# Performance work log

Hardware: AMD Instinct MI355X
Metric: run time of the kernel (lower is better)

## Reference

```python
import jax, jax.numpy as jnp
import numpy as np

B, N, C, R, E = 8, 4096, 128, 16, 65536


def setup_inputs() -> dict:
    key = jax.random.key(0)
    ks = jax.random.split(key, 8)
    node_features = jax.random.normal(ks[0], (B, N, C), dtype=jnp.float32)
    edge_index = jax.random.randint(ks[1], (B, 2, E), 0, N, dtype=jnp.int64)
    edge_type = jax.random.randint(ks[2], (B, E), 0, R, dtype=jnp.int64)
    s = 1.0 / np.sqrt(C)
    rel_weight = jax.random.uniform(ks[3], (R, C, C), jnp.float32, -s, s)
    root_weight = jax.random.uniform(ks[4], (C, C), jnp.float32, -s, s)
    rgcn_bias = jnp.zeros((C,), jnp.float32)
    lin_weight = jax.random.uniform(ks[5], (C, 1), jnp.float32, -s, s)
    lin_bias = jnp.zeros((1,), jnp.float32)
    return {
        'node_features': node_features,
        'edge_index': edge_index,
        'edge_type': edge_type,
        'rel_weight': rel_weight,
        'root_weight': root_weight,
        'rgcn_bias': rgcn_bias,
        'lin_weight': lin_weight,
        'lin_bias': lin_bias,
    }


def _rgcn_score(node_features, edge_index, edge_type, rel_weight, root_weight,
                rgcn_bias, lin_weight, lin_bias):
    # Flatten batch of graphs into one big disjoint graph (as batch_rgcn does).
    x = node_features.reshape(B * N, C)
    offs = (jnp.arange(B, dtype=edge_index.dtype) * N)[:, None, None]  # (B,1,1)
    ei = (edge_index + offs).transpose(1, 0, 2).reshape(2, B * E)  # (2, B*E)
    et = edge_type.reshape(B * E)
    src, dst = ei[0], ei[1]

    x_src = x[src]  # (B*E, C) gathered source features
    # root transform + bias (RGCNConv root_weight + bias)
    out = x @ root_weight + rgcn_bias  # (B*N, C)
    # per-relation mean aggregation; mean(W_r x_j) == W_r mean(x_j)
    for r in range(R):
        mask = (et == r).astype(x.dtype)  # (B*E,)
        s = jax.ops.segment_sum(x_src * mask[:, None], dst, num_segments=B * N)
        cnt = jax.ops.segment_sum(mask, dst, num_segments=B * N)
        mean = jnp.where(cnt[:, None] > 0, s / jnp.maximum(cnt, 1.0)[:, None], 0.0)
        out = out + mean @ rel_weight[r]

    out = jax.nn.relu(out)  # dropout is identity at eval
    scores = (out @ lin_weight + lin_bias).reshape(B, N)
    return scores


def reference(node_features, edge_index, edge_type, rel_weight, root_weight,
              rgcn_bias, lin_weight, lin_bias):
    return _rgcn_score(node_features, edge_index, edge_type, rel_weight,
                       root_weight, rgcn_bias, lin_weight, lin_bias)
```

## Files before the change

kernel.cpp:

```cpp
#include <hip/hip_runtime.h>

#define BB 8
#define NN 4096
#define CC 128
#define RR 16
#define EE 65536
#define NNODES 32768
#define NEDGES 524288
#define BCAP  48
#define SCAP  16
#define NT    32
#define ALP   136

typedef unsigned short ushort_t;
typedef short bf16x8 __attribute__((ext_vector_type(8)));
typedef float f32x4 __attribute__((ext_vector_type(4)));

__device__ __forceinline__ unsigned short f2b(float f) {
    unsigned u = __builtin_bit_cast(unsigned, f);
    unsigned r = (u + 0x7fffu + ((u >> 16) & 1u)) >> 16;
    return (unsigned short)r;
}
__device__ __forceinline__ float b2f(unsigned short s) {
    return __builtin_bit_cast(float, (unsigned)s << 16);
}
__device__ __forceinline__ float ldf(const void* p, int j, int isbf) {
    return isbf ? b2f(((const ushort_t*)p)[j]) : ((const float*)p)[j];
}
__device__ __forceinline__ int ldi(const int* p, int j, int is64) {
    return p[j << is64];
}
__device__ __forceinline__ unsigned cvtpk(float lo, float hi) {
    unsigned r;
    asm("v_cvt_pk_bf16_f32 %0, %1, %2" : "=v"(r) : "v"(lo), "v"(hi));
    return r;
}

__device__ __forceinline__ int probe_isbf(const ushort_t* xf) {
    int t = threadIdx.x & 63;
    int bad = 0;
    for (int j = t; j < 512; j += 64) {
        unsigned e = (xf[j] >> 7) & 0xffu;
        if (e >= 160u) bad = 1;
    }
    return __ballot(bad) == 0ull;
}

#define GATHER_SUM(u, sb) do { \
    s[sb+0] += __builtin_bit_cast(float, (u).x << 16); \
    s[sb+1] += __builtin_bit_cast(float, (u).x & 0xffff0000u); \
    s[sb+2] += __builtin_bit_cast(float, (u).y << 16); \
    s[sb+3] += __builtin_bit_cast(float, (u).y & 0xffff0000u); \
    s[sb+4] += __builtin_bit_cast(float, (u).z << 16); \
    s[sb+5] += __builtin_bit_cast(float, (u).z & 0xffff0000u); \
    s[sb+6] += __builtin_bit_cast(float, (u).w << 16); \
    s[sb+7] += __builtin_bit_cast(float, (u).w & 0xffff0000u); \
} while (0)

__global__ __launch_bounds__(256) void prep_k(const void* __restrict__ x,
                                              const void* __restrict__ relw,
                                              const void* __restrict__ rootw,
                                              const int* __restrict__ ei,
                                              const int* __restrict__ et,
                                              ushort_t* __restrict__ Xb,
                                              ushort_t* __restrict__ WT3,
                                              int* __restrict__ dcnt,
                                              int* __restrict__ bucket,
                                              int* __restrict__ flags) {
    int bx = blockIdx.x, t = threadIdx.x;
    if (bx < 512) {
        int lane = t & 63;
        int pa = (lane < 16) ? ei[2 * lane + 1] : 0;
        int pb = (lane < 16) ? et[2 * lane + 1] : 0;
        int w64i = (__ballot(pa != 0) == 0ull);
        int w64t = (__ballot(pb != 0) == 0ull);
        int b = bx & 7;
        #pragma unroll
        for (int i = 0; i < 4; ++i) {
            int e = (bx >> 3) * 1024 + i * 256 + t;
            int src = ldi(ei, (b * 2) * EE + e, w64i);
            int dst = ldi(ei, (b * 2 + 1) * EE + e, w64i);
            int r = ldi(et, (b << 16) + e, w64t);
            int gd = (b << 12) + dst;
            int pos = atomicAdd(&dcnt[gd], 1);
            if (pos < BCAP)
                bucket[gd * BCAP + pos] = (((b << 12) + src) << 4) | r;
        }
    } else if (bx < 1024) {
        int isbf = probe_isbf((const ushort_t*)x);
        int bx2 = bx - 512;
        int base = (bx2 & 7) * 65536 + (bx2 >> 3) * 256 + t;
        #pragma unroll
        for (int i = 0; i < 4; ++i) {
            int tid = base + i * 16384;
            if (isbf) {
                ((uint4*)Xb)[tid] = ((const uint4*)x)[tid];
            } else {
                const float4* xf = (const float4*)x;
                float4 a = xf[2 * tid], b = xf[2 * tid + 1];
                ushort4 o0, o1;
                o0.x = f2b(a.x); o0.y = f2b(a.y); o0.z = f2b(a.z); o0.w = f2b(a.w);
                o1.x = f2b(b.x); o1.y = f2b(b.y); o1.z = f2b(b.z); o1.w = f2b(b.w);
                ((ushort4*)Xb)[2 * tid] = o0; ((ushort4*)Xb)[2 * tid + 1] = o1;
            }
        }
    } else {
        __shared__ ushort_t Ls[128 * 40];
        int isbf = probe_isbf((const ushort_t*)x);
        int mb = bx - 1024;
        int mat = mb >> 2, chunk = mb & 3;
        const void* src = (mat == 16) ? rootw : relw;
        int soff = (mat == 16) ? 0 : mat * 16384;
        int k0 = chunk * 32;
        #pragma unroll
        for (int i = 0; i < 16; ++i) {
            int idx = t + i * 256;
            int k = idx >> 7, c = idx & 127;
            Ls[c * 40 + k] = f2b(ldf(src, soff + (k0 + k) * 128 + c, isbf));
        }
        __syncthreads();
        #pragma unroll
        for (int i = 0; i < 2; ++i) {
            int idx = t + i * 256;
            int cg = idx >> 6, lane = idx & 63;
            int lrow = lane & 15, lq = lane >> 4;
            uint4 v = *(const uint4*)(&Ls[(cg * 16 + lrow) * 40 + lq * 8]);
            *(uint4*)(WT3 + ((size_t)((mat * 4 + chunk) * 8 + cg)) * 512 + lane * 8) = v;
        }
        if (mb == 0 && t == 0) flags[0] = isbf;
    }
}

__global__ __launch_bounds__(256, 4) void agg_k(const ushort_t* __restrict__ Xb,
                                                const ushort_t* __restrict__ WT3,
                                                const int* __restrict__ dcnt,
                                                const int* __restrict__ bucket,
                                                const void* __restrict__ bias,
                                                const void* __restrict__ linw,
                                                const void* __restrict__ linb,
                                                void* __restrict__ out,
                                                const int* __restrict__ flags) {
    __shared__ int scnt[NT * 16];
    __shared__ ushort_t srt[NT * 16 * SCAP];
    __shared__ ushort_t A[2][NT * ALP];
    __shared__ float red[NT][5];
    int bx = blockIdx.x, t = threadIdx.x;
    int isbf = flags[0];
    int n0 = (bx & 7) * NN + (bx >> 3) * NT;

    scnt[t] = 0; scnt[256 + t] = 0;
    __syncthreads();

    int nsub = t >> 3, tsub = t & 7;
    int gn = n0 + nsub;
    int offA = tsub * 8, offB = 64 + tsub * 8;
    int nc = dcnt[gn]; if (nc > BCAP) nc = BCAP;
    const int* bk = bucket + gn * BCAP;
    for (int j = tsub; j < nc; j += 8) {
        int v = bk[j];
        int pos = atomicAdd(&scnt[(nsub << 4) + (v & 15)], 1);
        if (pos < SCAP)
            srt[(((nsub << 4) + (v & 15)) << 4) + pos] = (ushort_t)((unsigned)v >> 4);
    }
    __syncthreads();

    int wave = t >> 6, lane = t & 63, lrow = lane & 15, lq = lane >> 4;
    f32x4 acc[2][2] = {};

    {
        int cf = scnt[nsub << 4];
        int ce = cf > SCAP ? SCAP : cf;
        const ushort_t* lst = &srt[nsub << 8];
        float s[16];
        #pragma unroll
        for (int j = 0; j < 16; ++j) s[j] = 0.f;
        for (int e = 0; e < ce; ++e) {
            const ushort_t* xr = Xb + (size_t)lst[e] * 128;
            uint4 ua = *(const uint4*)(xr + offA), ub = *(const uint4*)(xr + offB);
            GATHER_SUM(ua, 0); GATHER_SUM(ub, 8);
        }
        float w = (cf > 0) ? 1.0f / (float)cf : 0.f;
        uint4 va, vb;
        va.x = cvtpk(s[0] * w, s[1] * w);   va.y = cvtpk(s[2] * w, s[3] * w);
        va.z = cvtpk(s[4] * w, s[5] * w);   va.w = cvtpk(s[6] * w, s[7] * w);
        vb.x = cvtpk(s[8] * w, s[9] * w);   vb.y = cvtpk(s[10] * w, s[11] * w);
        vb.z = cvtpk(s[12] * w, s[13] * w); vb.w = cvtpk(s[14] * w, s[15] * w);
        *(uint4*)(&A[0][nsub * ALP + offA]) = va;
        *(uint4*)(&A[0][nsub * ALP + offB]) = vb;
    }
    __syncthreads();

    for (int p = 0; p < 17; ++p) {
        int np = p + 1;
        uint4 r0a, r0b, r1a, r1b, r2a, r2b, r3a, r3b;
        int cf = 0, ce = 0;
        if (np < 16) {
            cf = scnt[(nsub << 4) + np];
            ce = cf > SCAP ? SCAP : cf;
            uint4 q0 = *(const uint4*)(&srt[((nsub << 4) + np) << 4]);
            int e0 = q0.x & 0xffffu, e1 = q0.x >> 16;
            int e2i = q0.y & 0xffffu, e3 = q0.y >> 16;
            if (ce > 0) { const ushort_t* xr = Xb + (size_t)e0 * 128;  r0a = *(const uint4*)(xr + offA); r0b = *(const uint4*)(xr + offB); }
            if (ce > 1) { const ushort_t* xr = Xb + (size_t)e1 * 128;  r1a = *(const uint4*)(xr + offA); r1b = *(const uint4*)(xr + offB); }
            if (ce > 2) { const ushort_t* xr = Xb + (size_t)e2i * 128; r2a = *(const uint4*)(xr + offA); r2b = *(const uint4*)(xr + offB); }
            if (ce > 3) { const ushort_t* xr = Xb + (size_t)e3 * 128;  r3a = *(const uint4*)(xr + offA); r3b = *(const uint4*)(xr + offB); }
        } else if (np == 16) {
            const ushort_t* xr = Xb + (size_t)gn * 128;
            r0a = *(const uint4*)(xr + offA); r0b = *(const uint4*)(xr + offB);
        }
        const ushort_t* Ap = A[p & 1];
        const ushort_t* bw = WT3 + (size_t)p * 16384 + (wave * 2) * 512 + lane * 8;
        __builtin_amdgcn_s_setprio(1);
        #pragma unroll
        for (int ks = 0; ks < 4; ++ks) {
            int k0 = ks * 32 + lq * 8;
            bf16x8 a0 = *(const bf16x8*)(&Ap[lrow * ALP + k0]);
            bf16x8 a1 = *(const bf16x8*)(&Ap[(16 + lrow) * ALP + k0]);
            bf16x8 b0 = *(const bf16x8*)(bw + ks * 4096);
            bf16x8 b1 = *(const bf16x8*)(bw + ks * 4096 + 512);
            acc[0][0] = __builtin_amdgcn_mfma_f32_16x16x32_bf16(a0, b0, acc[0][0], 0, 0, 0);
            acc[0][1] = __builtin_amdgcn_mfma_f32_16x16x32_bf16(a0, b1, acc[0][1], 0, 0, 0);
            acc[1][0] = __builtin_amdgcn_mfma_f32_16x16x32_bf16(a1, b0, acc[1][0], 0, 0, 0);
            acc[1][1] = __builtin_amdgcn_mfma_f32_16x16x32_bf16(a1, b1, acc[1][1], 0, 0, 0);
        }
        __builtin_amdgcn_s_setprio(0);
        if (np < 16) {
            float s[16];
            #pragma unroll
            for (int j = 0; j < 16; ++j) s[j] = 0.f;
            if (ce > 0) { GATHER_SUM(r0a, 0); GATHER_SUM(r0b, 8); }
            if (ce > 1) { GATHER_SUM(r1a, 0); GATHER_SUM(r1b, 8); }
            if (ce > 2) { GATHER_SUM(r2a, 0); GATHER_SUM(r2b, 8); }
            if (ce > 3) { GATHER_SUM(r3a, 0); GATHER_SUM(r3b, 8); }
            if (ce > 4) {
                const ushort_t* lst = &srt[((nsub << 4) + np) << 4];
                for (int e4 = 4; e4 < ce; ++e4) {
                    const ushort_t* xr = Xb + (size_t)lst[e4] * 128;
                    uint4 ta = *(const uint4*)(xr + offA), tb = *(const uint4*)(xr + offB);
                    GATHER_SUM(ta, 0); GATHER_SUM(tb, 8);
                }
            }
            float w = (cf > 0) ? 1.0f / (float)cf : 0.f;
            uint4 va, vb;
            va.x = cvtpk(s[0] * w, s[1] * w);   va.y = cvtpk(s[2] * w, s[3] * w);
            va.z = cvtpk(s[4] * w, s[5] * w);   va.w = cvtpk(s[6] * w, s[7] * w);
            vb.x = cvtpk(s[8] * w, s[9] * w);   vb.y = cvtpk(s[10] * w, s[11] * w);
            vb.z = cvtpk(s[12] * w, s[13] * w); vb.w = cvtpk(s[14] * w, s[15] * w);
            *(uint4*)(&A[np & 1][nsub * ALP + offA]) = va;
            *(uint4*)(&A[np & 1][nsub * ALP + offB]) = vb;
        } else if (np == 16) {
            *(uint4*)(&A[np & 1][nsub * ALP + offA]) = r0a;
            *(uint4*)(&A[np & 1][nsub * ALP + offB]) = r0b;
        }
        if (p < 16) __syncthreads();
    }

    int wn = wave << 5;
    int c0 = wn + lrow, c1 = wn + 16 + lrow;
    float bi0 = ldf(bias, c0, isbf), bi1 = ldf(bias, c1, isbf);
    float lw0 = ldf(linw, c0, isbf), lw1 = ldf(linw, c1, isbf);
    #pragma unroll
    for (int mi = 0; mi < 2; ++mi)
        #pragma unroll
        for (int rg = 0; rg < 4; ++rg) {
            float p = fmaxf(acc[mi][0][rg] + bi0, 0.f) * lw0
                    + fmaxf(acc[mi][1][rg] + bi1, 0.f) * lw1;
            p += __shfl_xor(p, 1, 64);
            p += __shfl_xor(p, 2, 64);
            p += __shfl_xor(p, 4, 64);
            p += __shfl_xor(p, 8, 64);
            if (lrow == 0) red[mi * 16 + lq * 4 + rg][wave] = p;
        }
    __syncthreads();
    if (t < NT) {
        float res = red[t][0] + red[t][1] + red[t][2] + red[t][3] + ldf(linb, 0, isbf);
        if (isbf) ((ushort_t*)out)[n0 + t] = f2b(res);
        else      ((float*)out)[n0 + t] = res;
    }
}

extern "C" void kernel_launch(void* const* d_in, const int* in_sizes, int n_in,
                              void* d_out, int out_size, void* d_ws, size_t ws_size,
                              hipStream_t stream) {
    const void* x     = d_in[0];
    const int*  ei    = (const int*)d_in[1];
    const int*  et    = (const int*)d_in[2];
    const void* relw  = d_in[3];
    const void* rootw = d_in[4];
    const void* bias  = d_in[5];
    const void* linw  = d_in[6];
    const void* linb  = d_in[7];

    const size_t WS_NEED = 15368448;
    if (ws_size < WS_NEED) return;

    char* ws = (char*)d_ws;
    ushort_t* Xb     = (ushort_t*)(ws);
    ushort_t* WT3    = (ushort_t*)(ws + 8388608);
    int*      dcnt   = (int*)(ws + 8945664);
    int*      bucket = (int*)(ws + 9076736);
    int*      flags  = (int*)(ws + 15368192);

    hipMemsetAsync(dcnt, 0, 131072, stream);
    prep_k<<<1092, 256, 0, stream>>>(x, relw, rootw, ei, et, Xb, WT3, dcnt, bucket, flags);
    agg_k<<<1024, 256, 0, stream>>>(Xb, WT3, dcnt, bucket, bias, linw, linb, d_out, flags);
}
```

Measured before the change: 144.4 us.

## Gather fp32 features directly and drop the bf16 copy pass

Removes the prep pass that converted the node features into a bf16 copy. The aggregation kernel now gathers fp32 rows straight from the input and converts to bf16 only after averaging, using a template that selects the dtype path. Input dtype and index width are now read from the input sizes on the host instead of being probed on the device. Each per-destination counter is padded to its own 64-byte slot to cut atomic contention, and each sorted-list count is stored inline with its list so one load fetches both. In exchange the gathers read twice the bytes per edge, and the kernel runs with lower launch-bound occupancy (3 instead of 4).

```diff
diff --git a/kernel.cpp b/kernel.cpp
--- a/kernel.cpp
+++ b/kernel.cpp
@@ -8,7 +8,7 @@
 #define NNODES 32768
 #define NEDGES 524288
 #define BCAP  48
-#define SCAP  16
+#define SCE   15
 #define NT    32
 #define ALP   136
 
@@ -36,17 +36,7 @@
     return r;
 }
 
-__device__ __forceinline__ int probe_isbf(const ushort_t* xf) {
-    int t = threadIdx.x & 63;
-    int bad = 0;
-    for (int j = t; j < 512; j += 64) {
-        unsigned e = (xf[j] >> 7) & 0xffu;
-        if (e >= 160u) bad = 1;
-    }
-    return __ballot(bad) == 0ull;
-}
-
-#define GATHER_SUM(u, sb) do { \
+#define GSUM_BF(u, sb) do { \
     s[sb+0] += __builtin_bit_cast(float, (u).x << 16); \
     s[sb+1] += __builtin_bit_cast(float, (u).x & 0xffff0000u); \
     s[sb+2] += __builtin_bit_cast(float, (u).y << 16); \
@@ -56,24 +46,20 @@
     s[sb+6] += __builtin_bit_cast(float, (u).w << 16); \
     s[sb+7] += __builtin_bit_cast(float, (u).w & 0xffff0000u); \
 } while (0)
-
-__global__ __launch_bounds__(256) void prep_k(const void* __restrict__ x,
-                                              const void* __restrict__ relw,
+#define GSUM_F4(f, sb) do { \
+    s[sb+0] += (f).x; s[sb+1] += (f).y; s[sb+2] += (f).z; s[sb+3] += (f).w; \
+} while (0)
+
+__global__ __launch_bounds__(256) void prep_k(const void* __restrict__ relw,
                                               const void* __restrict__ rootw,
                                               const int* __restrict__ ei,
                                               const int* __restrict__ et,
-                                              ushort_t* __restrict__ Xb,
                                               ushort_t* __restrict__ WT3,
                                               int* __restrict__ dcnt,
                                               int* __restrict__ bucket,
-                                              int* __restrict__ flags) {
+                                              int isbf, int w64i, int w64t) {
     int bx = blockIdx.x, t = threadIdx.x;
     if (bx < 512) {
-        int lane = t & 63;
-        int pa = (lane < 16) ? ei[2 * lane + 1] : 0;
-        int pb = (lane < 16) ? et[2 * lane + 1] : 0;
-        int w64i = (__ballot(pa != 0) == 0ull);
-        int w64t = (__ballot(pb != 0) == 0ull);
         int b = bx & 7;
         #pragma unroll
         for (int i = 0; i < 4; ++i) {
@@ -82,32 +68,13 @@
             int dst = ldi(ei, (b * 2 + 1) * EE + e, w64i);
             int r = ldi(et, (b << 16) + e, w64t);
             int gd = (b << 12) + dst;
-            int pos = atomicAdd(&dcnt[gd], 1);
+            int pos = atomicAdd(&dcnt[gd << 4], 1);
             if (pos < BCAP)
                 bucket[gd * BCAP + pos] = (((b << 12) + src) << 4) | r;
         }
-    } else if (bx < 1024) {
-        int isbf = probe_isbf((const ushort_t*)x);
-        int bx2 = bx - 512;
-        int base = (bx2 & 7) * 65536 + (bx2 >> 3) * 256 + t;
-        #pragma unroll
-        for (int i = 0; i < 4; ++i) {
-            int tid = base + i * 16384;
-            if (isbf) {
-                ((uint4*)Xb)[tid] = ((const uint4*)x)[tid];
-            } else {
-                const float4* xf = (const float4*)x;
-                float4 a = xf[2 * tid], b = xf[2 * tid + 1];
-                ushort4 o0, o1;
-                o0.x = f2b(a.x); o0.y = f2b(a.y); o0.z = f2b(a.z); o0.w = f2b(a.w);
-                o1.x = f2b(b.x); o1.y = f2b(b.y); o1.z = f2b(b.z); o1.w = f2b(b.w);
-                ((ushort4*)Xb)[2 * tid] = o0; ((ushort4*)Xb)[2 * tid + 1] = o1;
-            }
-        }
     } else {
         __shared__ ushort_t Ls[128 * 40];
-        int isbf = probe_isbf((const ushort_t*)x);
-        int mb = bx - 1024;
+        int mb = bx - 512;
         int mat = mb >> 2, chunk = mb & 3;
         const void* src = (mat == 16) ? rootw : relw;
         int soff = (mat == 16) ? 0 : mat * 16384;
@@ -127,25 +94,23 @@
             uint4 v = *(const uint4*)(&Ls[(cg * 16 + lrow) * 40 + lq * 8]);
             *(uint4*)(WT3 + ((size_t)((mat * 4 + chunk) * 8 + cg)) * 512 + lane * 8) = v;
         }
-        if (mb == 0 && t == 0) flags[0] = isbf;
-    }
-}
-
-__global__ __launch_bounds__(256, 4) void agg_k(const ushort_t* __restrict__ Xb,
+    }
+}
+
+template<int ISBF>
+__global__ __launch_bounds__(256, 3) void agg_t(const void* __restrict__ x,
                                                 const ushort_t* __restrict__ WT3,
                                                 const int* __restrict__ dcnt,
                                                 const int* __restrict__ bucket,
                                                 const void* __restrict__ bias,
                                                 const void* __restrict__ linw,
                                                 const void* __restrict__ linb,
-                                                void* __restrict__ out,
-                                                const int* __restrict__ flags) {
+                                                void* __restrict__ out) {
     __shared__ int scnt[NT * 16];
-    __shared__ ushort_t srt[NT * 16 * SCAP];
+    __shared__ ushort_t srt[NT * 16 * 16];
     __shared__ ushort_t A[2][NT * ALP];
     __shared__ float red[NT][5];
     int bx = blockIdx.x, t = threadIdx.x;
-    int isbf = flags[0];
     int n0 = (bx & 7) * NN + (bx >> 3) * NT;
 
     scnt[t] = 0; scnt[256 + t] = 0;
@@ -154,30 +119,43 @@
     int nsub = t >> 3, tsub = t & 7;
     int gn = n0 + nsub;
     int offA = tsub * 8, offB = 64 + tsub * 8;
-    int nc = dcnt[gn]; if (nc > BCAP) nc = BCAP;
+    int nc = dcnt[gn << 4]; if (nc > BCAP) nc = BCAP;
     const int* bk = bucket + gn * BCAP;
     for (int j = tsub; j < nc; j += 8) {
         int v = bk[j];
-        int pos = atomicAdd(&scnt[(nsub << 4) + (v & 15)], 1);
-        if (pos < SCAP)
-            srt[(((nsub << 4) + (v & 15)) << 4) + pos] = (ushort_t)((unsigned)v >> 4);
-    }
-    __syncthreads();
-
+        int row = (nsub << 4) + (v & 15);
+        int pos = atomicAdd(&scnt[row], 1);
+        if (pos < SCE)
+            srt[(row << 4) + 1 + pos] = (ushort_t)((unsigned)v >> 4);
+    }
+    __syncthreads();
+    srt[t << 4] = (ushort_t)scnt[t];
+    srt[(t + 256) << 4] = (ushort_t)scnt[t + 256];
+    __syncthreads();
+
+    const ushort_t* xh = (const ushort_t*)x;
+    const float4* xf = (const float4*)x;
     int wave = t >> 6, lane = t & 63, lrow = lane & 15, lq = lane >> 4;
     f32x4 acc[2][2] = {};
 
     {
-        int cf = scnt[nsub << 4];
-        int ce = cf > SCAP ? SCAP : cf;
-        const ushort_t* lst = &srt[nsub << 8];
+        int row = nsub << 4;
+        uint4 q0 = *(const uint4*)(&srt[row << 4]);
+        int cf = q0.x & 0xffffu; int ce = cf > SCE ? SCE : cf;
         float s[16];
         #pragma unroll
         for (int j = 0; j < 16; ++j) s[j] = 0.f;
         for (int e = 0; e < ce; ++e) {
-            const ushort_t* xr = Xb + (size_t)lst[e] * 128;
-            uint4 ua = *(const uint4*)(xr + offA), ub = *(const uint4*)(xr + offB);
-            GATHER_SUM(ua, 0); GATHER_SUM(ub, 8);
+            int gs = srt[(row << 4) + 1 + e];
+            if (ISBF) {
+                const ushort_t* xr = xh + (size_t)gs * 128;
+                uint4 ua = *(const uint4*)(xr + offA), ub = *(const uint4*)(xr + offB);
+                GSUM_BF(ua, 0); GSUM_BF(ub, 8);
+            } else {
+                const float4* xr = xf + (size_t)gs * 32 + tsub * 2;
+                float4 a0 = xr[0], a1 = xr[1], b0 = xr[16], b1 = xr[17];
+                GSUM_F4(a0, 0); GSUM_F4(a1, 4); GSUM_F4(b0, 8); GSUM_F4(b1, 12);
+            }
         }
         float w = (cf > 0) ? 1.0f / (float)cf : 0.f;
         uint4 va, vb;
@@ -193,20 +171,33 @@
     for (int p = 0; p < 17; ++p) {
         int np = p + 1;
         uint4 r0a, r0b, r1a, r1b, r2a, r2b, r3a, r3b;
-        int cf = 0, ce = 0;
+        float4 f0a, f0b, f0c, f0d, f1a, f1b, f1c, f1d;
+        float4 f2a, f2b_, f2c, f2d, f3a, f3b_, f3c, f3d;
+        int cf = 0, ce = 0, row = 0;
         if (np < 16) {
-            cf = scnt[(nsub << 4) + np];
-            ce = cf > SCAP ? SCAP : cf;
-            uint4 q0 = *(const uint4*)(&srt[((nsub << 4) + np) << 4]);
-            int e0 = q0.x & 0xffffu, e1 = q0.x >> 16;
-            int e2i = q0.y & 0xffffu, e3 = q0.y >> 16;
-            if (ce > 0) { const ushort_t* xr = Xb + (size_t)e0 * 128;  r0a = *(const uint4*)(xr + offA); r0b = *(const uint4*)(xr + offB); }
-            if (ce > 1) { const ushort_t* xr = Xb + (size_t)e1 * 128;  r1a = *(const uint4*)(xr + offA); r1b = *(const uint4*)(xr + offB); }
-            if (ce > 2) { const ushort_t* xr = Xb + (size_t)e2i * 128; r2a = *(const uint4*)(xr + offA); r2b = *(const uint4*)(xr + offB); }
-            if (ce > 3) { const ushort_t* xr = Xb + (size_t)e3 * 128;  r3a = *(const uint4*)(xr + offA); r3b = *(const uint4*)(xr + offB); }
+            row = (nsub << 4) + np;
+            uint4 q0 = *(const uint4*)(&srt[row << 4]);
+            cf = q0.x & 0xffffu; ce = cf > SCE ? SCE : cf;
+            int e0 = q0.x >> 16, e1 = q0.y & 0xffffu, e2 = q0.y >> 16, e3 = q0.z & 0xffffu;
+            if (ISBF) {
+                if (ce > 0) { const ushort_t* xr = xh + (size_t)e0 * 128; r0a = *(const uint4*)(xr + offA); r0b = *(const uint4*)(xr + offB); }
+                if (ce > 1) { const ushort_t* xr = xh + (size_t)e1 * 128; r1a = *(const uint4*)(xr + offA); r1b = *(const uint4*)(xr + offB); }
+                if (ce > 2) { const ushort_t* xr = xh + (size_t)e2 * 128; r2a = *(const uint4*)(xr + offA); r2b = *(const uint4*)(xr + offB); }
+                if (ce > 3) { const ushort_t* xr = xh + (size_t)e3 * 128; r3a = *(const uint4*)(xr + offA); r3b = *(const uint4*)(xr + offB); }
+            } else {
+                if (ce > 0) { const float4* xr = xf + (size_t)e0 * 32 + tsub * 2; f0a = xr[0]; f0b = xr[1]; f0c = xr[16]; f0d = xr[17]; }
+                if (ce > 1) { const float4* xr = xf + (size_t)e1 * 32 + tsub * 2; f1a = xr[0]; f1b = xr[1]; f1c = xr[16]; f1d = xr[17]; }
+                if (ce > 2) { const float4* xr = xf + (size_t)e2 * 32 + tsub * 2; f2a = xr[0]; f2b_ = xr[1]; f2c = xr[16]; f2d = xr[17]; }
+                if (ce > 3) { const float4* xr = xf + (size_t)e3 * 32 + tsub * 2; f3a = xr[0]; f3b_ = xr[1]; f3c = xr[16]; f3d = xr[17]; }
+            }
         } else if (np == 16) {
-            const ushort_t* xr = Xb + (size_t)gn * 128;
-            r0a = *(const uint4*)(xr + offA); r0b = *(const uint4*)(xr + offB);
+            if (ISBF) {
+                const ushort_t* xr = xh + (size_t)gn * 128;
+                r0a = *(const uint4*)(xr + offA); r0b = *(const uint4*)(xr + offB);
+            } else {
+                const float4* xr = xf + (size_t)gn * 32 + tsub * 2;
+                f0a = xr[0]; f0b = xr[1]; f0c = xr[16]; f0d = xr[17];
+            }
         }
         const ushort_t* Ap = A[p & 1];
         const ushort_t* bw = WT3 + (size_t)p * 16384 + (wave * 2) * 512 + lane * 8;
@@ -228,16 +219,29 @@
             float s[16];
             #pragma unroll
             for (int j = 0; j < 16; ++j) s[j] = 0.f;
-            if (ce > 0) { GATHER_SUM(r0a, 0); GATHER_SUM(r0b, 8); }
-            if (ce > 1) { GATHER_SUM(r1a, 0); GATHER_SUM(r1b, 8); }
-            if (ce > 2) { GATHER_SUM(r2a, 0); GATHER_SUM(r2b, 8); }
-            if (ce > 3) { GATHER_SUM(r3a, 0); GATHER_SUM(r3b, 8); }
+            if (ISBF) {
+                if (ce > 0) { GSUM_BF(r0a, 0); GSUM_BF(r0b, 8); }
+                if (ce > 1) { GSUM_BF(r1a, 0); GSUM_BF(r1b, 8); }
+                if (ce > 2) { GSUM_BF(r2a, 0); GSUM_BF(r2b, 8); }
+                if (ce > 3) { GSUM_BF(r3a, 0); GSUM_BF(r3b, 8); }
+            } else {
+                if (ce > 0) { GSUM_F4(f0a, 0); GSUM_F4(f0b, 4); GSUM_F4(f0c, 8); GSUM_F4(f0d, 12); }
+                if (ce > 1) { GSUM_F4(f1a, 0); GSUM_F4(f1b, 4); GSUM_F4(f1c, 8); GSUM_F4(f1d, 12); }
+                if (ce > 2) { GSUM_F4(f2a, 0); GSUM_F4(f2b_, 4); GSUM_F4(f2c, 8); GSUM_F4(f2d, 12); }
+                if (ce > 3) { GSUM_F4(f3a, 0); GSUM_F4(f3b_, 4); GSUM_F4(f3c, 8); GSUM_F4(f3d, 12); }
+            }
             if (ce > 4) {
-                const ushort_t* lst = &srt[((nsub << 4) + np) << 4];
                 for (int e4 = 4; e4 < ce; ++e4) {
-                    const ushort_t* xr = Xb + (size_t)lst[e4] * 128;
-                    uint4 ta = *(const uint4*)(xr + offA), tb = *(const uint4*)(xr + offB);
-                    GATHER_SUM(ta, 0); GATHER_SUM(tb, 8);
+                    int gs = srt[(row << 4) + 1 + e4];
+                    if (ISBF) {
+                        const ushort_t* xr = xh + (size_t)gs * 128;
+                        uint4 ta = *(const uint4*)(xr + offA), tb = *(const uint4*)(xr + offB);
+                        GSUM_BF(ta, 0); GSUM_BF(tb, 8);
+                    } else {
+                        const float4* xr = xf + (size_t)gs * 32 + tsub * 2;
+                        float4 ta = xr[0], tb = xr[1], tc = xr[16], td = xr[17];
+                        GSUM_F4(ta, 0); GSUM_F4(tb, 4); GSUM_F4(tc, 8); GSUM_F4(td, 12);
+                    }
                 }
             }
             float w = (cf > 0) ? 1.0f / (float)cf : 0.f;
@@ -249,16 +253,24 @@
             *(uint4*)(&A[np & 1][nsub * ALP + offA]) = va;
             *(uint4*)(&A[np & 1][nsub * ALP + offB]) = vb;
         } else if (np == 16) {
-            *(uint4*)(&A[np & 1][nsub * ALP + offA]) = r0a;
-            *(uint4*)(&A[np & 1][nsub * ALP + offB]) = r0b;
+            uint4 va, vb;
+            if (ISBF) { va = r0a; vb = r0b; }
+            else {
+                va.x = cvtpk(f0a.x, f0a.y); va.y = cvtpk(f0a.z, f0a.w);
+                va.z = cvtpk(f0b.x, f0b.y); va.w = cvtpk(f0b.z, f0b.w);
+                vb.x = cvtpk(f0c.x, f0c.y); vb.y = cvtpk(f0c.z, f0c.w);
+                vb.z = cvtpk(f0d.x, f0d.y); vb.w = cvtpk(f0d.z, f0d.w);
+            }
+            *(uint4*)(&A[np & 1][nsub * ALP + offA]) = va;
+            *(uint4*)(&A[np & 1][nsub * ALP + offB]) = vb;
         }
         if (p < 16) __syncthreads();
     }
 
     int wn = wave << 5;
     int c0 = wn + lrow, c1 = wn + 16 + lrow;
-    float bi0 = ldf(bias, c0, isbf), bi1 = ldf(bias, c1, isbf);
-    float lw0 = ldf(linw, c0, isbf), lw1 = ldf(linw, c1, isbf);
+    float bi0 = ldf(bias, c0, ISBF), bi1 = ldf(bias, c1, ISBF);
+    float lw0 = ldf(linw, c0, ISBF), lw1 = ldf(linw, c1, ISBF);
     #pragma unroll
     for (int mi = 0; mi < 2; ++mi)
         #pragma unroll
@@ -273,8 +285,8 @@
         }
     __syncthreads();
     if (t < NT) {
-        float res = red[t][0] + red[t][1] + red[t][2] + red[t][3] + ldf(linb, 0, isbf);
-        if (isbf) ((ushort_t*)out)[n0 + t] = f2b(res);
+        float res = red[t][0] + red[t][1] + red[t][2] + red[t][3] + ldf(linb, 0, ISBF);
+        if (ISBF) ((ushort_t*)out)[n0 + t] = f2b(res);
         else      ((float*)out)[n0 + t] = res;
     }
 }
@@ -291,17 +303,22 @@
     const void* linw  = d_in[6];
     const void* linb  = d_in[7];
 
-    const size_t WS_NEED = 15368448;
+    int isbf = (in_sizes[0] == BB * NN * CC * 2);
+    int w64i = (in_sizes[1] == BB * 2 * EE * 8);
+    int w64t = (in_sizes[2] == BB * EE * 8);
+
+    const size_t WS_NEED = 8945664;
     if (ws_size < WS_NEED) return;
 
     char* ws = (char*)d_ws;
-    ushort_t* Xb     = (ushort_t*)(ws);
-    ushort_t* WT3    = (ushort_t*)(ws + 8388608);
-    int*      dcnt   = (int*)(ws + 8945664);
-    int*      bucket = (int*)(ws + 9076736);
-    int*      flags  = (int*)(ws + 15368192);
-
-    hipMemsetAsync(dcnt, 0, 131072, stream);
-    prep_k<<<1092, 256, 0, stream>>>(x, relw, rootw, ei, et, Xb, WT3, dcnt, bucket, flags);
-    agg_k<<<1024, 256, 0, stream>>>(Xb, WT3, dcnt, bucket, bias, linw, linb, d_out, flags);
-}
+    ushort_t* WT3    = (ushort_t*)(ws);
+    int*      dcnt   = (int*)(ws + 557056);
+    int*      bucket = (int*)(ws + 2654208);
+
+    hipMemsetAsync(dcnt, 0, 2097152, stream);
+    prep_k<<<580, 256, 0, stream>>>(relw, rootw, ei, et, WT3, dcnt, bucket, isbf, w64i, w64t);
+    if (isbf)
+        agg_t<1><<<1024, 256, 0, stream>>>(x, WT3, dcnt, bucket, bias, linw, linb, d_out);
+    else
+        agg_t<0><<<1024, 256, 0, stream>>>(x, WT3, dcnt, bucket, bias, linw, linb, d_out);
+}
```

After: 174.1 us. 1.21x slower.

## Halve node tile per block, pad degree counters, and move type detection to host

Applied to the files above, without the earlier changes.

The aggregation kernel now handles 16 nodes per block instead of 32, with 16 threads per node each gathering 8 channels, and launches twice as many blocks at higher occupancy. Per-relation counts are stored inline in the sorted-source list so a single LDS vector read yields the count and the first indices. The per-destination counters are spaced 64 bytes apart to reduce atomic contention, and the edge-bucketing work is spread over more blocks. Input dtype and index-width detection move from device probes to host size checks. In exchange, each block does half the MFMA work per weight-tile load, so B-matrix traffic per node doubles, and the memset grows larger.

```diff
diff --git a/kernel.cpp b/kernel.cpp
--- a/kernel.cpp
+++ b/kernel.cpp
@@ -8,8 +8,8 @@
 #define NNODES 32768
 #define NEDGES 524288
 #define BCAP  48
-#define SCAP  16
-#define NT    32
+#define SCE   15
+#define NT    16
 #define ALP   136
 
 typedef unsigned short ushort_t;
@@ -36,25 +36,15 @@
     return r;
 }
 
-__device__ __forceinline__ int probe_isbf(const ushort_t* xf) {
-    int t = threadIdx.x & 63;
-    int bad = 0;
-    for (int j = t; j < 512; j += 64) {
-        unsigned e = (xf[j] >> 7) & 0xffu;
-        if (e >= 160u) bad = 1;
-    }
-    return __ballot(bad) == 0ull;
-}
-
-#define GATHER_SUM(u, sb) do { \
-    s[sb+0] += __builtin_bit_cast(float, (u).x << 16); \
-    s[sb+1] += __builtin_bit_cast(float, (u).x & 0xffff0000u); \
-    s[sb+2] += __builtin_bit_cast(float, (u).y << 16); \
-    s[sb+3] += __builtin_bit_cast(float, (u).y & 0xffff0000u); \
-    s[sb+4] += __builtin_bit_cast(float, (u).z << 16); \
-    s[sb+5] += __builtin_bit_cast(float, (u).z & 0xffff0000u); \
-    s[sb+6] += __builtin_bit_cast(float, (u).w << 16); \
-    s[sb+7] += __builtin_bit_cast(float, (u).w & 0xffff0000u); \
+#define GSUM8(u) do { \
+    s[0] += __builtin_bit_cast(float, (u).x << 16); \
+    s[1] += __builtin_bit_cast(float, (u).x & 0xffff0000u); \
+    s[2] += __builtin_bit_cast(float, (u).y << 16); \
+    s[3] += __builtin_bit_cast(float, (u).y & 0xffff0000u); \
+    s[4] += __builtin_bit_cast(float, (u).z << 16); \
+    s[5] += __builtin_bit_cast(float, (u).z & 0xffff0000u); \
+    s[6] += __builtin_bit_cast(float, (u).w << 16); \
+    s[7] += __builtin_bit_cast(float, (u).w & 0xffff0000u); \
 } while (0)
 
 __global__ __launch_bounds__(256) void prep_k(const void* __restrict__ x,
@@ -66,29 +56,23 @@
                                               ushort_t* __restrict__ WT3,
                                               int* __restrict__ dcnt,
                                               int* __restrict__ bucket,
-                                              int* __restrict__ flags) {
+                                              int isbf, int w64i, int w64t) {
     int bx = blockIdx.x, t = threadIdx.x;
-    if (bx < 512) {
-        int lane = t & 63;
-        int pa = (lane < 16) ? ei[2 * lane + 1] : 0;
-        int pb = (lane < 16) ? et[2 * lane + 1] : 0;
-        int w64i = (__ballot(pa != 0) == 0ull);
-        int w64t = (__ballot(pb != 0) == 0ull);
+    if (bx < 1024) {
         int b = bx & 7;
         #pragma unroll
-        for (int i = 0; i < 4; ++i) {
-            int e = (bx >> 3) * 1024 + i * 256 + t;
+        for (int i = 0; i < 2; ++i) {
+            int e = (bx >> 3) * 512 + i * 256 + t;
             int src = ldi(ei, (b * 2) * EE + e, w64i);
             int dst = ldi(ei, (b * 2 + 1) * EE + e, w64i);
             int r = ldi(et, (b << 16) + e, w64t);
             int gd = (b << 12) + dst;
-            int pos = atomicAdd(&dcnt[gd], 1);
+            int pos = atomicAdd(&dcnt[gd << 4], 1);
             if (pos < BCAP)
                 bucket[gd * BCAP + pos] = (((b << 12) + src) << 4) | r;
         }
-    } else if (bx < 1024) {
-        int isbf = probe_isbf((const ushort_t*)x);
-        int bx2 = bx - 512;
+    } else if (bx < 1536) {
+        int bx2 = bx - 1024;
         int base = (bx2 & 7) * 65536 + (bx2 >> 3) * 256 + t;
         #pragma unroll
         for (int i = 0; i < 4; ++i) {
@@ -106,8 +90,7 @@
         }
     } else {
         __shared__ ushort_t Ls[128 * 40];
-        int isbf = probe_isbf((const ushort_t*)x);
-        int mb = bx - 1024;
+        int mb = bx - 1536;
         int mat = mb >> 2, chunk = mb & 3;
         const void* src = (mat == 16) ? rootw : relw;
         int soff = (mat == 16) ? 0 : mat * 16384;
@@ -127,11 +110,10 @@
             uint4 v = *(const uint4*)(&Ls[(cg * 16 + lrow) * 40 + lq * 8]);
             *(uint4*)(WT3 + ((size_t)((mat * 4 + chunk) * 8 + cg)) * 512 + lane * 8) = v;
         }
-        if (mb == 0 && t == 0) flags[0] = isbf;
-    }
-}
-
-__global__ __launch_bounds__(256, 4) void agg_k(const ushort_t* __restrict__ Xb,
+    }
+}
+
+__global__ __launch_bounds__(256, 6) void agg_k(const ushort_t* __restrict__ Xb,
                                                 const ushort_t* __restrict__ WT3,
                                                 const int* __restrict__ dcnt,
                                                 const int* __restrict__ bucket,
@@ -139,74 +121,71 @@
                                                 const void* __restrict__ linw,
                                                 const void* __restrict__ linb,
                                                 void* __restrict__ out,
-                                                const int* __restrict__ flags) {
+                                                int isbf) {
     __shared__ int scnt[NT * 16];
-    __shared__ ushort_t srt[NT * 16 * SCAP];
+    __shared__ ushort_t srt[NT * 16 * 16];
     __shared__ ushort_t A[2][NT * ALP];
     __shared__ float red[NT][5];
     int bx = blockIdx.x, t = threadIdx.x;
-    int isbf = flags[0];
     int n0 = (bx & 7) * NN + (bx >> 3) * NT;
 
-    scnt[t] = 0; scnt[256 + t] = 0;
-    __syncthreads();
-
-    int nsub = t >> 3, tsub = t & 7;
+    scnt[t] = 0;
+    __syncthreads();
+
+    int nsub = t >> 4, tsub = t & 15;
     int gn = n0 + nsub;
-    int offA = tsub * 8, offB = 64 + tsub * 8;
-    int nc = dcnt[gn]; if (nc > BCAP) nc = BCAP;
+    int offA = tsub * 8;
+    int nc = dcnt[gn << 4]; if (nc > BCAP) nc = BCAP;
     const int* bk = bucket + gn * BCAP;
-    for (int j = tsub; j < nc; j += 8) {
+    for (int j = tsub; j < nc; j += 16) {
         int v = bk[j];
-        int pos = atomicAdd(&scnt[(nsub << 4) + (v & 15)], 1);
-        if (pos < SCAP)
-            srt[(((nsub << 4) + (v & 15)) << 4) + pos] = (ushort_t)((unsigned)v >> 4);
-    }
+        int row = (nsub << 4) + (v & 15);
+        int pos = atomicAdd(&scnt[row], 1);
+        if (pos < SCE)
+            srt[(row << 4) + 1 + pos] = (ushort_t)((unsigned)v >> 4);
+    }
+    __syncthreads();
+    srt[t << 4] = (ushort_t)scnt[t];
     __syncthreads();
 
     int wave = t >> 6, lane = t & 63, lrow = lane & 15, lq = lane >> 4;
-    f32x4 acc[2][2] = {};
+    f32x4 acc0 = {}, acc1 = {};
 
     {
-        int cf = scnt[nsub << 4];
-        int ce = cf > SCAP ? SCAP : cf;
-        const ushort_t* lst = &srt[nsub << 8];
-        float s[16];
-        #pragma unroll
-        for (int j = 0; j < 16; ++j) s[j] = 0.f;
+        int row = nsub << 4;
+        uint4 q0 = *(const uint4*)(&srt[row << 4]);
+        int cf = q0.x & 0xffffu; int ce = cf > SCE ? SCE : cf;
+        float s[8];
+        #pragma unroll
+        for (int j = 0; j < 8; ++j) s[j] = 0.f;
         for (int e = 0; e < ce; ++e) {
-            const ushort_t* xr = Xb + (size_t)lst[e] * 128;
-            uint4 ua = *(const uint4*)(xr + offA), ub = *(const uint4*)(xr + offB);
-            GATHER_SUM(ua, 0); GATHER_SUM(ub, 8);
+            int gs = srt[(row << 4) + 1 + e];
+            uint4 u = *(const uint4*)(Xb + (size_t)gs * 128 + offA);
+            GSUM8(u);
         }
         float w = (cf > 0) ? 1.0f / (float)cf : 0.f;
-        uint4 va, vb;
-        va.x = cvtpk(s[0] * w, s[1] * w);   va.y = cvtpk(s[2] * w, s[3] * w);
-        va.z = cvtpk(s[4] * w, s[5] * w);   va.w = cvtpk(s[6] * w, s[7] * w);
-        vb.x = cvtpk(s[8] * w, s[9] * w);   vb.y = cvtpk(s[10] * w, s[11] * w);
-        vb.z = cvtpk(s[12] * w, s[13] * w); vb.w = cvtpk(s[14] * w, s[15] * w);
+        uint4 va;
+        va.x = cvtpk(s[0] * w, s[1] * w); va.y = cvtpk(s[2] * w, s[3] * w);
+        va.z = cvtpk(s[4] * w, s[5] * w); va.w = cvtpk(s[6] * w, s[7] * w);
         *(uint4*)(&A[0][nsub * ALP + offA]) = va;
-        *(uint4*)(&A[0][nsub * ALP + offB]) = vb;
     }
     __syncthreads();
 
     for (int p = 0; p < 17; ++p) {
         int np = p + 1;
-        uint4 r0a, r0b, r1a, r1b, r2a, r2b, r3a, r3b;
-        int cf = 0, ce = 0;
+        uint4 r0, r1, r2, r3;
+        int cf = 0, ce = 0, row = 0;
         if (np < 16) {
-            cf = scnt[(nsub << 4) + np];
-            ce = cf > SCAP ? SCAP : cf;
-            uint4 q0 = *(const uint4*)(&srt[((nsub << 4) + np) << 4]);
-            int e0 = q0.x & 0xffffu, e1 = q0.x >> 16;
-            int e2i = q0.y & 0xffffu, e3 = q0.y >> 16;
-            if (ce > 0) { const ushort_t* xr = Xb + (size_t)e0 * 128;  r0a = *(const uint4*)(xr + offA); r0b = *(const uint4*)(xr + offB); }
-            if (ce > 1) { const ushort_t* xr = Xb + (size_t)e1 * 128;  r1a = *(const uint4*)(xr + offA); r1b = *(const uint4*)(xr + offB); }
-            if (ce > 2) { const ushort_t* xr = Xb + (size_t)e2i * 128; r2a = *(const uint4*)(xr + offA); r2b = *(const uint4*)(xr + offB); }
-            if (ce > 3) { const ushort_t* xr = Xb + (size_t)e3 * 128;  r3a = *(const uint4*)(xr + offA); r3b = *(const uint4*)(xr + offB); }
+            row = (nsub << 4) + np;
+            uint4 q0 = *(const uint4*)(&srt[row << 4]);
+            cf = q0.x & 0xffffu; ce = cf > SCE ? SCE : cf;
+            int e0 = q0.x >> 16, e1 = q0.y & 0xffffu, e2 = q0.y >> 16, e3 = q0.z & 0xffffu;
+            if (ce > 0) r0 = *(const uint4*)(Xb + (size_t)e0 * 128 + offA);
+            if (ce > 1) r1 = *(const uint4*)(Xb + (size_t)e1 * 128 + offA);
+            if (ce > 2) r2 = *(const uint4*)(Xb + (size_t)e2 * 128 + offA);
+            if (ce > 3) r3 = *(const uint4*)(Xb + (size_t)e3 * 128 + offA);
         } else if (np == 16) {
-            const ushort_t* xr = Xb + (size_t)gn * 128;
-            r0a = *(const uint4*)(xr + offA); r0b = *(const uint4*)(xr + offB);
+            r0 = *(const uint4*)(Xb + (size_t)gn * 128 + offA);
         }
         const ushort_t* Ap = A[p & 1];
         const ushort_t* bw = WT3 + (size_t)p * 16384 + (wave * 2) * 512 + lane * 8;
@@ -215,42 +194,34 @@
         for (int ks = 0; ks < 4; ++ks) {
             int k0 = ks * 32 + lq * 8;
             bf16x8 a0 = *(const bf16x8*)(&Ap[lrow * ALP + k0]);
-            bf16x8 a1 = *(const bf16x8*)(&Ap[(16 + lrow) * ALP + k0]);
             bf16x8 b0 = *(const bf16x8*)(bw + ks * 4096);
             bf16x8 b1 = *(const bf16x8*)(bw + ks * 4096 + 512);
-            acc[0][0] = __builtin_amdgcn_mfma_f32_16x16x32_bf16(a0, b0, acc[0][0], 0, 0, 0);
-            acc[0][1] = __builtin_amdgcn_mfma_f32_16x16x32_bf16(a0, b1, acc[0][1], 0, 0, 0);
-            acc[1][0] = __builtin_amdgcn_mfma_f32_16x16x32_bf16(a1, b0, acc[1][0], 0, 0, 0);
-            acc[1][1] = __builtin_amdgcn_mfma_f32_16x16x32_bf16(a1, b1, acc[1][1], 0, 0, 0);
+            acc0 = __builtin_amdgcn_mfma_f32_16x16x32_bf16(a0, b0, acc0, 0, 0, 0);
+            acc1 = __builtin_amdgcn_mfma_f32_16x16x32_bf16(a0, b1, acc1, 0, 0, 0);
         }
         __builtin_amdgcn_s_setprio(0);
         if (np < 16) {
-            float s[16];
+            float s[8];
             #pragma unroll
-            for (int j = 0; j < 16; ++j) s[j] = 0.f;
-            if (ce > 0) { GATHER_SUM(r0a, 0); GATHER_SUM(r0b, 8); }
-            if (ce > 1) { GATHER_SUM(r1a, 0); GATHER_SUM(r1b, 8); }
-            if (ce > 2) { GATHER_SUM(r2a, 0); GATHER_SUM(r2b, 8); }
-            if (ce > 3) { GATHER_SUM(r3a, 0); GATHER_SUM(r3b, 8); }
+            for (int j = 0; j < 8; ++j) s[j] = 0.f;
+            if (ce > 0) GSUM8(r0);
+            if (ce > 1) GSUM8(r1);
+            if (ce > 2) GSUM8(r2);
+            if (ce > 3) GSUM8(r3);
             if (ce > 4) {
-                const ushort_t* lst = &srt[((nsub << 4) + np) << 4];
                 for (int e4 = 4; e4 < ce; ++e4) {
-                    const ushort_t* xr = Xb + (size_t)lst[e4] * 128;
-                    uint4 ta = *(const uint4*)(xr + offA), tb = *(const uint4*)(xr + offB);
-                    GATHER_SUM(ta, 0); GATHER_SUM(tb, 8);
+                    int gs = srt[(row << 4) + 1 + e4];
+                    uint4 u = *(const uint4*)(Xb + (size_t)gs * 128 + offA);
+                    GSUM8(u);
                 }
             }
             float w = (cf > 0) ? 1.0f / (float)cf : 0.f;
-            uint4 va, vb;
-            va.x = cvtpk(s[0] * w, s[1] * w);   va.y = cvtpk(s[2] * w, s[3] * w);
-            va.z = cvtpk(s[4] * w, s[5] * w);   va.w = cvtpk(s[6] * w, s[7] * w);
-            vb.x = cvtpk(s[8] * w, s[9] * w);   vb.y = cvtpk(s[10] * w, s[11] * w);
-            vb.z = cvtpk(s[12] * w, s[13] * w); vb.w = cvtpk(s[14] * w, s[15] * w);
+            uint4 va;
+            va.x = cvtpk(s[0] * w, s[1] * w); va.y = cvtpk(s[2] * w, s[3] * w);
+            va.z = cvtpk(s[4] * w, s[5] * w); va.w = cvtpk(s[6] * w, s[7] * w);
             *(uint4*)(&A[np & 1][nsub * ALP + offA]) = va;
-            *(uint4*)(&A[np & 1][nsub * ALP + offB]) = vb;
         } else if (np == 16) {
-            *(uint4*)(&A[np & 1][nsub * ALP + offA]) = r0a;
-            *(uint4*)(&A[np & 1][nsub * ALP + offB]) = r0b;
+            *(uint4*)(&A[np & 1][nsub * ALP + offA]) = r0;
         }
         if (p < 16) __syncthreads();
     }
@@ -260,17 +231,15 @@
     float bi0 = ldf(bias, c0, isbf), bi1 = ldf(bias, c1, isbf);
     float lw0 = ldf(linw, c0, isbf), lw1 = ldf(linw, c1, isbf);
     #pragma unroll
-    for (int mi = 0; mi < 2; ++mi)
-        #pragma unroll
-        for (int rg = 0; rg < 4; ++rg) {
-            float p = fmaxf(acc[mi][0][rg] + bi0, 0.f) * lw0
-                    + fmaxf(acc[mi][1][rg] + bi1, 0.f) * lw1;
-            p += __shfl_xor(p, 1, 64);
-            p += __shfl_xor(p, 2, 64);
-            p += __shfl_xor(p, 4, 64);
-            p += __shfl_xor(p, 8, 64);
-            if (lrow == 0) red[mi * 16 + lq * 4 + rg][wave] = p;
-        }
+    for (int rg = 0; rg < 4; ++rg) {
+        float p = fmaxf(acc0[rg] + bi0, 0.f) * lw0
+                + fmaxf(acc1[rg] + bi1, 0.f) * lw1;
+        p += __shfl_xor(p, 1, 64);
+        p += __shfl_xor(p, 2, 64);
+        p += __shfl_xor(p, 4, 64);
+        p += __shfl_xor(p, 8, 64);
+        if (lrow == 0) red[lq * 4 + rg][wave] = p;
+    }
     __syncthreads();
     if (t < NT) {
         float res = red[t][0] + red[t][1] + red[t][2] + red[t][3] + ldf(linb, 0, isbf);
@@ -291,17 +260,21 @@
     const void* linw  = d_in[6];
     const void* linb  = d_in[7];
 
-    const size_t WS_NEED = 15368448;
+    int isbf = (in_sizes[0] == BB * NN * CC * 2);
+    int w64i = (in_sizes[1] == BB * 2 * EE * 8);
+    int w64t = (in_sizes[2] == BB * EE * 8);
+
+    const size_t WS_NEED = 17334272;
     if (ws_size < WS_NEED) return;
 
     char* ws = (char*)d_ws;
     ushort_t* Xb     = (ushort_t*)(ws);
     ushort_t* WT3    = (ushort_t*)(ws + 8388608);
     int*      dcnt   = (int*)(ws + 8945664);
-    int*      bucket = (int*)(ws + 9076736);
-    int*      flags  = (int*)(ws + 15368192);
-
-    hipMemsetAsync(dcnt, 0, 131072, stream);
-    prep_k<<<1092, 256, 0, stream>>>(x, relw, rootw, ei, et, Xb, WT3, dcnt, bucket, flags);
-    agg_k<<<1024, 256, 0, stream>>>(Xb, WT3, dcnt, bucket, bias, linw, linb, d_out, flags);
-}
+    int*      bucket = (int*)(ws + 11042816);
+
+    hipMemsetAsync(dcnt, 0, 2097152, stream);
+    prep_k<<<1604, 256, 0, stream>>>(x, relw, rootw, ei, et, Xb, WT3, dcnt, bucket,
+                                     isbf, w64i, w64t);
+    agg_k<<<2048, 256, 0, stream>>>(Xb, WT3, dcnt, bucket, bias, linw, linb, d_out, isbf);
+}
```

New measurement: 163.4 us. 1.13x slower.
